# Optimization experiments

Hardware: AMD Instinct MI355X
Metric: run time of the kernel (lower is better)

Reference implementation:

```python
import jax, jax.numpy as jnp
import numpy as np

N_TOKENS = 8192
IN_FEATURES = 4096
OUT_FEATURES = 4096


def setup_inputs() -> dict:
    key = jax.random.key(0)
    kx, kw, ks = jax.random.split(key, 3)
    x = jax.random.normal(kx, (N_TOKENS, IN_FEATURES), dtype=jnp.float32)
    # int8 weight in [-127, 126], per torch.randint(-127, 127, ...)
    weight = jax.random.randint(kw, (OUT_FEATURES, IN_FEATURES), -127, 127, dtype=jnp.int32).astype(jnp.int8)
    weight_scales = jax.random.uniform(ks, (OUT_FEATURES,), dtype=jnp.float32, minval=0.001, maxval=0.01)
    bias = jnp.zeros((1, OUT_FEATURES), dtype=jnp.float32)
    return {"x": x, "weight": weight, "weight_scales": weight_scales, "bias": bias}


def reference(x, weight, weight_scales, bias):
    # --- dynamic per-token activation quantization (min-max / abs-max) ---
    # scale per token so that max |x| maps to 127
    x_absmax = jnp.max(jnp.abs(x), axis=-1, keepdims=True)          # [T, 1]
    x_scale = x_absmax / 127.0                                       # [T, 1]
    q_x = jnp.clip(jnp.round(x / x_scale), -127, 127).astype(jnp.int8)  # [T, K]

    # --- int8 GEMM with int32 accumulation: q_y = q_x @ weight.T ---
    q_y = jax.lax.dot_general(
        q_x, weight,
        dimension_numbers=(((1,), (1,)), ((), ())),
        preferred_element_type=jnp.int32,
    )                                                                # [T, N] int32

    # --- dequantize: per-channel weight scale x per-token activation scale ---
    y = q_y.astype(jnp.float32) * weight_scales[None, :] * x_scale   # [T, N]
    y = y + bias
    return y
```

## Files before the change

### kernel.cpp

```cpp
#include <hip/hip_runtime.h>
#include <cstdint>
#include <cstddef>

#define T_TOKENS 8192
#define K_DIM 4096
#define N_DIM 4096

using i32x4 = __attribute__((ext_vector_type(4))) int;

__global__ __launch_bounds__(256) void pack_weight(const int* __restrict__ win,
                                                   int8_t* __restrict__ wout) {
    const int idx = blockIdx.x * 256 + threadIdx.x;
    const i32x4 v = reinterpret_cast<const i32x4*>(win)[idx];
    uint32_t pk = (uint32_t)(v.x & 255) | ((uint32_t)(v.y & 255) << 8) |
                  ((uint32_t)(v.z & 255) << 16) | ((uint32_t)(v.w & 255) << 24);
    reinterpret_cast<int*>(wout)[idx] = (int)pk;
}

__global__ __launch_bounds__(256) void quant_rows(const float* __restrict__ x,
                                                  int8_t* __restrict__ qx,
                                                  float* __restrict__ xscale) {
    const int t = blockIdx.x;
    const int tid = threadIdx.x;
    const float4* row = reinterpret_cast<const float4*>(x + (size_t)t * K_DIM);

    float4 v[4];
    float amax = 0.0f;
#pragma unroll
    for (int i = 0; i < 4; ++i) {
        v[i] = row[i * 256 + tid];
        amax = fmaxf(amax, fabsf(v[i].x));
        amax = fmaxf(amax, fabsf(v[i].y));
        amax = fmaxf(amax, fabsf(v[i].z));
        amax = fmaxf(amax, fabsf(v[i].w));
    }
#pragma unroll
    for (int off = 32; off > 0; off >>= 1)
        amax = fmaxf(amax, __shfl_xor(amax, off));

    __shared__ float red[4];
    if ((tid & 63) == 0) red[tid >> 6] = amax;
    __syncthreads();
    amax = fmaxf(fmaxf(red[0], red[1]), fmaxf(red[2], red[3]));

    const float scale = fmaxf(amax, 1e-30f) * (1.0f / 127.0f);
    if (tid == 0) xscale[t] = scale;

    int* qrow = reinterpret_cast<int*>(qx + (size_t)t * K_DIM);
#pragma unroll
    for (int i = 0; i < 4; ++i) {
        int q0 = (int)fminf(fmaxf(rintf(v[i].x / scale), -127.0f), 127.0f);
        int q1 = (int)fminf(fmaxf(rintf(v[i].y / scale), -127.0f), 127.0f);
        int q2 = (int)fminf(fmaxf(rintf(v[i].z / scale), -127.0f), 127.0f);
        int q3 = (int)fminf(fmaxf(rintf(v[i].w / scale), -127.0f), 127.0f);
        uint32_t pk = (uint32_t)(q0 & 255) | ((uint32_t)(q1 & 255) << 8) |
                      ((uint32_t)(q2 & 255) << 16) | ((uint32_t)(q3 & 255) << 24);
        qrow[i * 256 + tid] = (int)pk;
    }
}

__global__ __launch_bounds__(256) void int8_gemm(const int8_t* __restrict__ qx,
                                                 const int8_t* __restrict__ w,
                                                 const float* __restrict__ xscale,
                                                 const float* __restrict__ wscale,
                                                 const float* __restrict__ bias,
                                                 float* __restrict__ out) {
    __shared__ int8_t As[128 * 64];
    __shared__ int8_t Bs[128 * 64];

    const int tid = threadIdx.x;
    const int lane = tid & 63;
    const int wave = tid >> 6;
    const int wr = wave >> 1;
    const int wc = wave & 1;
    const int l16 = lane & 15;
    const int quad = lane >> 4;

    const size_t a_row0 = (size_t)blockIdx.x * 128;
    const size_t b_row0 = (size_t)blockIdx.y * 128;

    const int s_row = tid >> 2;
    const int s_col = (tid & 3) * 16;

    const int8_t* ag0 = qx + (a_row0 + s_row) * (size_t)K_DIM + s_col;
    const int8_t* ag1 = ag0 + (size_t)64 * K_DIM;
    const int8_t* bg0 = w + (b_row0 + s_row) * (size_t)K_DIM + s_col;
    const int8_t* bg1 = bg0 + (size_t)64 * K_DIM;

    i32x4* As4 = reinterpret_cast<i32x4*>(As);
    i32x4* Bs4 = reinterpret_cast<i32x4*>(Bs);

    i32x4 acc[4][4] = {};

    i32x4 ra0 = *reinterpret_cast<const i32x4*>(ag0);
    i32x4 ra1 = *reinterpret_cast<const i32x4*>(ag1);
    i32x4 rb0 = *reinterpret_cast<const i32x4*>(bg0);
    i32x4 rb1 = *reinterpret_cast<const i32x4*>(bg1);

    for (int k0 = 0; k0 < K_DIM; k0 += 64) {
        __syncthreads();
        As4[tid] = ra0;
        As4[tid + 256] = ra1;
        Bs4[tid] = rb0;
        Bs4[tid + 256] = rb1;
        __syncthreads();

        const int k1 = k0 + 64;
        if (k1 < K_DIM) {
            ra0 = *reinterpret_cast<const i32x4*>(ag0 + k1);
            ra1 = *reinterpret_cast<const i32x4*>(ag1 + k1);
            rb0 = *reinterpret_cast<const i32x4*>(bg0 + k1);
            rb1 = *reinterpret_cast<const i32x4*>(bg1 + k1);
        }

        i32x4 af[4], bf[4];
#pragma unroll
        for (int i = 0; i < 4; ++i) {
            af[i] = As4[((wr * 64 + i * 16 + l16) * 64 + quad * 16) >> 4];
            bf[i] = Bs4[((wc * 64 + i * 16 + l16) * 64 + quad * 16) >> 4];
        }
#pragma unroll
        for (int i = 0; i < 4; ++i)
#pragma unroll
            for (int j = 0; j < 4; ++j)
                acc[i][j] = __builtin_amdgcn_mfma_i32_16x16x64_i8(af[i], bf[j], acc[i][j], 0, 0, 0);
    }

#pragma unroll
    for (int j = 0; j < 4; ++j) {
        const int n = (int)b_row0 + wc * 64 + j * 16 + l16;
        const float ws = wscale[n];
        const float bs = bias[n];
#pragma unroll
        for (int i = 0; i < 4; ++i) {
#pragma unroll
            for (int r = 0; r < 4; ++r) {
                const int t = (int)a_row0 + wr * 64 + i * 16 + quad * 4 + r;
                const float xs = xscale[t];
                out[(size_t)t * N_DIM + n] = (float)acc[i][j][r] * ws * xs + bs;
            }
        }
    }
}

extern "C" void kernel_launch(void* const* d_in, const int* in_sizes, int n_in,
                              void* d_out, int out_size, void* d_ws, size_t ws_size,
                              hipStream_t stream) {
    const float* x = (const float*)d_in[0];
    const int* w_i32 = (const int*)d_in[1];
    const float* wscale = (const float*)d_in[2];
    const float* bias = (const float*)d_in[3];
    float* out = (float*)d_out;

    int8_t* qx = (int8_t*)d_ws;
    float* xscale = (float*)((char*)d_ws + (size_t)T_TOKENS * K_DIM);
    int8_t* wpk = (int8_t*)((char*)d_ws + (size_t)T_TOKENS * K_DIM + 65536);

    pack_weight<<<(N_DIM * K_DIM / 4) / 256, 256, 0, stream>>>(w_i32, wpk);

    quant_rows<<<T_TOKENS, 256, 0, stream>>>(x, qx, xscale);

    dim3 grid(T_TOKENS / 128, N_DIM / 128);
    int8_gemm<<<grid, 256, 0, stream>>>(qx, wpk, xscale, wscale, bias, out);
}
```

Baseline: 474.8 us.

## Fuse prep kernels and rebuild int8 GEMM with direct-to-LDS double buffering

Weight packing and activation quantization are merged into one launch, which saves a kernel launch. The GEMM now uses 256x128 tiles with 512 threads. Tiles are staged through double-buffered global_load_lds with XOR-swizzled LDS columns, so loads overlap the MFMA work and LDS bank conflicts drop. A remapped 1D block index groups tiles across the XCDs for better L2 locality, and s_setprio raises priority around the MFMA section. The hand-written waitcnt counts and the swizzle mapping are fragile, and the larger tile raises register pressure.

```diff
diff --git a/kernel.cpp b/kernel.cpp
--- a/kernel.cpp
+++ b/kernel.cpp
@@ -6,22 +6,29 @@
 #define K_DIM 4096
 #define N_DIM 4096
 
+#define PACK_BLOCKS (N_DIM * K_DIM / 4 / 256)
+#define QUANT_BLOCKS T_TOKENS
+
 using i32x4 = __attribute__((ext_vector_type(4))) int;
 
-__global__ __launch_bounds__(256) void pack_weight(const int* __restrict__ win,
-                                                   int8_t* __restrict__ wout) {
-    const int idx = blockIdx.x * 256 + threadIdx.x;
-    const i32x4 v = reinterpret_cast<const i32x4*>(win)[idx];
-    uint32_t pk = (uint32_t)(v.x & 255) | ((uint32_t)(v.y & 255) << 8) |
-                  ((uint32_t)(v.z & 255) << 16) | ((uint32_t)(v.w & 255) << 24);
-    reinterpret_cast<int*>(wout)[idx] = (int)pk;
-}
+__global__ __launch_bounds__(256) void prep(const int* __restrict__ win,
+                                            int8_t* __restrict__ wout,
+                                            const float* __restrict__ x,
+                                            int8_t* __restrict__ qx,
+                                            float* __restrict__ xscale) {
+    const int bid = blockIdx.x;
+    const int tid = threadIdx.x;
 
-__global__ __launch_bounds__(256) void quant_rows(const float* __restrict__ x,
-                                                  int8_t* __restrict__ qx,
-                                                  float* __restrict__ xscale) {
-    const int t = blockIdx.x;
-    const int tid = threadIdx.x;
+    if (bid < PACK_BLOCKS) {
+        const int idx = bid * 256 + tid;
+        const i32x4 v = reinterpret_cast<const i32x4*>(win)[idx];
+        uint32_t pk = (uint32_t)(v.x & 255) | ((uint32_t)(v.y & 255) << 8) |
+                      ((uint32_t)(v.z & 255) << 16) | ((uint32_t)(v.w & 255) << 24);
+        reinterpret_cast<int*>(wout)[idx] = (int)pk;
+        return;
+    }
+
+    const int t = bid - PACK_BLOCKS;
     const float4* row = reinterpret_cast<const float4*>(x + (size_t)t * K_DIM);
 
     float4 v[4];
@@ -59,88 +66,112 @@
     }
 }
 
-__global__ __launch_bounds__(256) void int8_gemm(const int8_t* __restrict__ qx,
-                                                 const int8_t* __restrict__ w,
-                                                 const float* __restrict__ xscale,
-                                                 const float* __restrict__ wscale,
-                                                 const float* __restrict__ bias,
-                                                 float* __restrict__ out) {
-    __shared__ int8_t As[128 * 64];
-    __shared__ int8_t Bs[128 * 64];
+__global__ __launch_bounds__(512, 4) void int8_gemm(const int8_t* __restrict__ qx,
+                                                    const int8_t* __restrict__ w,
+                                                    const float* __restrict__ xscale,
+                                                    const float* __restrict__ wscale,
+                                                    const float* __restrict__ bias,
+                                                    float* __restrict__ out) {
+    __shared__ int8_t lds[49152];
 
     const int tid = threadIdx.x;
     const int lane = tid & 63;
     const int wave = tid >> 6;
     const int wr = wave >> 1;
-    const int wc = wave & 1;
+    const int wn = wave & 1;
     const int l16 = lane & 15;
     const int quad = lane >> 4;
 
-    const size_t a_row0 = (size_t)blockIdx.x * 128;
-    const size_t b_row0 = (size_t)blockIdx.y * 128;
+    const int bid = (int)blockIdx.x;
+    const int wg = ((bid & 7) << 7) | (bid >> 3);
+    const int tm = wg >> 5;
+    const int tn = wg & 31;
 
     const int s_row = tid >> 2;
-    const int s_col = (tid & 3) * 16;
+    const int scol = (((tid & 3) ^ ((s_row >> 1) & 3)) << 4);
+    const int fcol = ((quad ^ ((l16 >> 1) & 3)) << 4);
 
-    const int8_t* ag0 = qx + (a_row0 + s_row) * (size_t)K_DIM + s_col;
-    const int8_t* ag1 = ag0 + (size_t)64 * K_DIM;
-    const int8_t* bg0 = w + (b_row0 + s_row) * (size_t)K_DIM + s_col;
-    const int8_t* bg1 = bg0 + (size_t)64 * K_DIM;
+    const int8_t* pA = qx + (size_t)(tm * 256 + s_row) * K_DIM + scol;
+    const int8_t* pB = w + (size_t)(tn * 128 + s_row) * K_DIM + scol;
 
-    i32x4* As4 = reinterpret_cast<i32x4*>(As);
-    i32x4* Bs4 = reinterpret_cast<i32x4*>(Bs);
+    const int aoff = (wr * 64 + l16) * 64 + fcol;
+    const int boff = 16384 + (wn * 64 + l16) * 64 + fcol;
 
     i32x4 acc[4][4] = {};
+    i32x4 af[4], bf[4];
 
-    i32x4 ra0 = *reinterpret_cast<const i32x4*>(ag0);
-    i32x4 ra1 = *reinterpret_cast<const i32x4*>(ag1);
-    i32x4 rb0 = *reinterpret_cast<const i32x4*>(bg0);
-    i32x4 rb1 = *reinterpret_cast<const i32x4*>(bg1);
+#define GLOAD(gp, lp)                                              \
+    __builtin_amdgcn_global_load_lds(                              \
+        (const __attribute__((address_space(1))) void*)(gp),       \
+        (__attribute__((address_space(3))) void*)(lp), 16, 0, 0)
 
-    for (int k0 = 0; k0 < K_DIM; k0 += 64) {
-        __syncthreads();
-        As4[tid] = ra0;
-        As4[tid + 256] = ra1;
-        Bs4[tid] = rb0;
-        Bs4[tid + 256] = rb1;
-        __syncthreads();
-
-        const int k1 = k0 + 64;
-        if (k1 < K_DIM) {
-            ra0 = *reinterpret_cast<const i32x4*>(ag0 + k1);
-            ra1 = *reinterpret_cast<const i32x4*>(ag1 + k1);
-            rb0 = *reinterpret_cast<const i32x4*>(bg0 + k1);
-            rb1 = *reinterpret_cast<const i32x4*>(bg1 + k1);
-        }
-
-        i32x4 af[4], bf[4];
-#pragma unroll
-        for (int i = 0; i < 4; ++i) {
-            af[i] = As4[((wr * 64 + i * 16 + l16) * 64 + quad * 16) >> 4];
-            bf[i] = Bs4[((wc * 64 + i * 16 + l16) * 64 + quad * 16) >> 4];
-        }
-#pragma unroll
-        for (int i = 0; i < 4; ++i)
-#pragma unroll
-            for (int j = 0; j < 4; ++j)
-                acc[i][j] = __builtin_amdgcn_mfma_i32_16x16x64_i8(af[i], bf[j], acc[i][j], 0, 0, 0);
+#define STAGE(buf, kk)                                             \
+    {                                                              \
+        int8_t* l_ = lds + (buf) * 24576 + tid * 16;               \
+        GLOAD(pA + (kk), l_);                                      \
+        GLOAD(pA + (size_t)128 * K_DIM + (kk), l_ + 8192);         \
+        GLOAD(pB + (kk), l_ + 16384);                              \
     }
 
+#define READS(buf)                                                             \
+    {                                                                          \
+        const int8_t* sa_ = lds + (buf) * 24576 + aoff;                        \
+        const int8_t* sb_ = lds + (buf) * 24576 + boff;                        \
+        _Pragma("unroll") for (int q = 0; q < 4; ++q)                          \
+            af[q] = *(const i32x4*)(sa_ + q * 1024);                           \
+        _Pragma("unroll") for (int nj = 0; nj < 4; ++nj)                       \
+            bf[nj] = *(const i32x4*)(sb_ + nj * 1024);                         \
+    }
+
+#define MFMAS()                                                                \
+    __builtin_amdgcn_s_setprio(1);                                             \
+    _Pragma("unroll") for (int q = 0; q < 4; ++q) {                            \
+        _Pragma("unroll") for (int nj = 0; nj < 4; ++nj)                       \
+            acc[q][nj] = __builtin_amdgcn_mfma_i32_16x16x64_i8(                \
+                af[q], bf[nj], acc[q][nj], 0, 0, 0);                           \
+    }                                                                          \
+    __builtin_amdgcn_s_setprio(0);
+
+    STAGE(0, 0)
+
+    for (int t = 0; t < 63; ++t) {
+        const int cur = t & 1;
+        STAGE(cur ^ 1, (t + 1) << 6)
+        asm volatile("s_waitcnt vmcnt(3)" ::: "memory");
+        __builtin_amdgcn_s_barrier();
+        READS(cur)
+        MFMAS()
+        __builtin_amdgcn_s_barrier();
+    }
+    asm volatile("s_waitcnt vmcnt(0)" ::: "memory");
+    __builtin_amdgcn_s_barrier();
+    READS(1)
+    MFMAS()
+
+    const int rowb = tm * 256 + wr * 64 + quad * 4;
+    const int colb = tn * 128 + wn * 64 + l16;
+    float wsv[4], bsv[4];
 #pragma unroll
-    for (int j = 0; j < 4; ++j) {
-        const int n = (int)b_row0 + wc * 64 + j * 16 + l16;
-        const float ws = wscale[n];
-        const float bs = bias[n];
+    for (int nj = 0; nj < 4; ++nj) {
+        wsv[nj] = wscale[colb + nj * 16];
+        bsv[nj] = bias[colb + nj * 16];
+    }
 #pragma unroll
-        for (int i = 0; i < 4; ++i) {
+    for (int q = 0; q < 4; ++q) {
 #pragma unroll
-            for (int r = 0; r < 4; ++r) {
-                const int t = (int)a_row0 + wr * 64 + i * 16 + quad * 4 + r;
-                const float xs = xscale[t];
-                out[(size_t)t * N_DIM + n] = (float)acc[i][j][r] * ws * xs + bs;
-            }
+        for (int r = 0; r < 4; ++r) {
+            const int trow = rowb + q * 16 + r;
+            const float xs = xscale[trow];
+            float* orow = out + (size_t)trow * N_DIM + colb;
+#pragma unroll
+            for (int nj = 0; nj < 4; ++nj)
+                orow[nj * 16] = (float)acc[q][nj][r] * (wsv[nj] * xs) + bsv[nj];
         }
     }
+#undef GLOAD
+#undef STAGE
+#undef READS
+#undef MFMAS
 }
 
 extern "C" void kernel_launch(void* const* d_in, const int* in_sizes, int n_in,
@@ -156,10 +187,7 @@
     float* xscale = (float*)((char*)d_ws + (size_t)T_TOKENS * K_DIM);
     int8_t* wpk = (int8_t*)((char*)d_ws + (size_t)T_TOKENS * K_DIM + 65536);
 
-    pack_weight<<<(N_DIM * K_DIM / 4) / 256, 256, 0, stream>>>(w_i32, wpk);
+    prep<<<PACK_BLOCKS + QUANT_BLOCKS, 256, 0, stream>>>(w_i32, wpk, x, qx, xscale);
 
-    quant_rows<<<T_TOKENS, 256, 0, stream>>>(x, qx, xscale);
-
-    dim3 grid(T_TOKENS / 128, N_DIM / 128);
-    int8_gemm<<<grid, 256, 0, stream>>>(qx, wpk, xscale, wscale, bias, out);
+    int8_gemm<<<dim3(1024), dim3(512), 0, stream>>>(qx, wpk, xscale, wscale, bias, out);
 }
```

New measurement: 400.8 us. -15.6%, faster.
